# Optimization experiments

Measured on AMD Instinct MI355X. Metric: run time of the kernel, lower is better.

## Reference

```python
import jax, jax.numpy as jnp
import numpy as np

B, C, P, H, W = 8, 256, 64, 64, 64


def conv2d(x, w, b, pad):
    y = jax.lax.conv_general_dilated(
        x, w, window_strides=(1, 1), padding=[(pad, pad), (pad, pad)],
        dimension_numbers=("NCHW", "OIHW", "NCHW"))
    return y + b[None, :, None, None]


def setup_inputs() -> dict:
    key = jax.random.key(0)
    ks = jax.random.split(key, 9)
    x = jax.random.normal(ks[0], (B, C, H, W), dtype=jnp.float32)
    # conv weights, OIHW layout; scale ~ kaiming-ish
    w_top = jax.random.normal(ks[1], (P, C, 1, 1), jnp.float32) * (1.0 / np.sqrt(C))
    b_top = jnp.zeros((P,), jnp.float32)
    w_center = jax.random.normal(ks[2], (P, C, 1, 1), jnp.float32) * (1.0 / np.sqrt(C))
    b_center = jnp.zeros((P,), jnp.float32)
    w_bottom = jax.random.normal(ks[3], (C, C, 3, 3), jnp.float32) * (1.0 / np.sqrt(9 * C))
    b_bottom = jnp.zeros((C,), jnp.float32)
    w_out = jax.random.normal(ks[4], (C, C, 3, 3), jnp.float32) * (1.0 / np.sqrt(9 * C))
    b_out = jnp.zeros((C,), jnp.float32)
    return {"x": x, "w_top": w_top, "b_top": b_top, "w_center": w_center,
            "b_center": b_center, "w_bottom": w_bottom, "b_bottom": b_bottom,
            "w_out": w_out, "b_out": b_out}


def reference(x, w_top, b_top, w_center, b_center, w_bottom, b_bottom, w_out, b_out):
    b, c, h, w = x.shape
    hw = h * w
    x_top = conv2d(x, w_top, b_top, 0).reshape(b, -1, hw)          # [B, P, HW]
    x_center = conv2d(x, w_center, b_center, 0).reshape(b, -1, hw)  # [B, P, HW]
    x_center = jnp.swapaxes(x_center, 1, 2)                          # [B, HW, P]
    x_bottom = conv2d(x, w_bottom, b_bottom, 1).reshape(b, c, hw)
    x_bottom = jnp.swapaxes(x_bottom, 1, 2)                          # [B, HW, C]
    sp_map = jnp.einsum("bnp,bpm->bnm", x_center, x_top)            # [B, HW, HW]
    # NOTE: softmax is GLOBAL over the flattened HW*HW map per batch element,
    # not per-row (faithful to original Softmax(dim=1) on view(bsize, -1)).
    sp_map = jax.nn.softmax(sp_map.reshape(b, -1), axis=1).reshape(b, hw, hw)
    sp_map = jnp.einsum("bnm,bmc->bnc", sp_map, x_bottom)           # [B, HW, C]
    # NOTE: original does .reshape(b, C, h, w) on a [B, HW, C] tensor (no
    # transpose) -- replicate that exact memory reinterpretation.
    sp_map = sp_map.reshape(b, c, h, w)
    return conv2d(x + sp_map, w_out, b_out, 1)
```

## Files before the change

kernel.cpp:

```cpp
#include <hip/hip_runtime.h>
#include <hip/hip_bf16.h>
#include <type_traits>

constexpr int B_ = 8, C_ = 256, P_ = 64, H_ = 64, W_ = 64, HW_ = 4096;

typedef __attribute__((ext_vector_type(8))) short short8;
typedef __attribute__((ext_vector_type(4))) short short4v;
typedef __attribute__((ext_vector_type(4))) float f32x4;

__device__ __forceinline__ short bfbits(float f) {
    __hip_bfloat16 h = __float2bfloat16(f);
    return *reinterpret_cast<short*>(&h);
}
__device__ __forceinline__ float bf2f(short s) {
    __hip_bfloat16 h = *reinterpret_cast<__hip_bfloat16*>(&s);
    return (float)h;
}

#define GLL16(gsrc, ldst)                                                      \
    __builtin_amdgcn_global_load_lds(                                         \
        (const __attribute__((address_space(1))) void*)(gsrc),                \
        (__attribute__((address_space(3))) void*)(ldst), 16, 0, 0)


__global__ __launch_bounds__(256) void k_prep_w(
    const float* __restrict__ w, short8* __restrict__ wbP)
{
    const int idx = blockIdx.x * 256 + threadIdx.x;
    const int lane = idx & 63, cot = (idx >> 6) & 15;
    const int cb = (idx >> 10) & 7, tap = idx >> 13;
    const int lm = lane & 15, lq = lane >> 4;
    const int co = cot * 16 + lm, ci0 = cb * 32 + lq * 8;
    short8 v;
#pragma unroll
    for (int k = 0; k < 8; ++k)
        v[k] = bfbits(w[(co * 256 + ci0 + k) * 9 + tap]);
    wbP[idx] = v;
}

__global__ __launch_bounds__(256) void k_pack_xb(
    const __hip_bfloat16* __restrict__ xb, short8* __restrict__ xbP)
{
    const int tid = blockIdx.x * 256 + threadIdx.x;
    const int lane = tid & 63, wid = tid >> 6;
    const int ct = wid & 15, g = (wid >> 4) & 127, b = wid >> 11;
    const int c = ct * 16 + (lane >> 2);
    const int mo = g * 32 + (lane & 3) * 8;
    const short8 v = *reinterpret_cast<const short8*>(
        &xb[((size_t)(b * 256 + c)) * HW_ + mo]);
    xbP[(size_t)wid * 64 + (lane & 3) * 16 + (lane >> 2)] = v;
}

__global__ __launch_bounds__(256) void k_conv1x1(
    const float* __restrict__ x,
    const float* __restrict__ w_top, const float* __restrict__ b_top,
    const float* __restrict__ w_cen, const float* __restrict__ b_cen,
    short8* __restrict__ xtPh, short8* __restrict__ xtPl,
    short8* __restrict__ xcPh, short8* __restrict__ xcPl)
{
    const int b = blockIdx.z;
    const int n = blockIdx.x * 256 + threadIdx.x;
    const int conv = blockIdx.y >> 2, pq = blockIdx.y & 3;
    const int p0 = pq * 16;
    const float* w    = conv ? w_cen : w_top;
    const float* bias = conv ? b_cen : b_top;
    short8* oh = conv ? xcPh : xtPh;
    short8* ol = conv ? xcPl : xtPl;

    const float* xp = x + (size_t)b * C_ * HW_ + n;
    float acc[16];
#pragma unroll
    for (int p = 0; p < 16; ++p) acc[p] = 0.f;

    for (int c = 0; c < C_; c += 4) {
        const float xv0 = xp[(size_t)(c + 0) * HW_];
        const float xv1 = xp[(size_t)(c + 1) * HW_];
        const float xv2 = xp[(size_t)(c + 2) * HW_];
        const float xv3 = xp[(size_t)(c + 3) * HW_];
#pragma unroll
        for (int p = 0; p < 16; ++p) {
            const float4 wv = *reinterpret_cast<const float4*>(&w[(p0 + p) * C_ + c]);
            float a = acc[p];
            a = fmaf(wv.x, xv0, a);
            a = fmaf(wv.y, xv1, a);
            a = fmaf(wv.z, xv2, a);
            a = fmaf(wv.w, xv3, a);
            acc[p] = a;
        }
    }
    const int nt = n >> 4, lmn = n & 15;
    const size_t obase = ((size_t)(b * 256 + nt) * 2 + (pq >> 1)) * 64 + lmn;
#pragma unroll
    for (int jj = 0; jj < 2; ++jj) {
        short8 vh, vl;
#pragma unroll
        for (int k = 0; k < 8; ++k) {
            const float v = acc[jj * 8 + k] + bias[p0 + jj * 8 + k];
            const short hb = bfbits(v);
            vh[k] = hb;
            vl[k] = bfbits(v - bf2f(hb));
        }
        const size_t idx = obase + (size_t)(((pq & 1) * 2 + jj) * 16);
        oh[idx] = vh;
        ol[idx] = vl;
    }
}

template <typename OT>
__global__ __launch_bounds__(256) void k_conv3x3_mfma(
    const float* __restrict__ xin, const short8* __restrict__ wbP,
    const float* __restrict__ bias, OT* __restrict__ out)
{
    __shared__ __align__(16) __hip_bfloat16 Xs[3][66][40];
    const int b = blockIdx.z, h = blockIdx.x, cohalf = blockIdx.y;
    const int t = threadIdx.x;
    const int wave = t >> 6, lane = t & 63;
    const int lm = lane & 15, lq = lane >> 4;
    const int cobase = cohalf * 128 + wave * 32;
    const int cot0 = cohalf * 8 + wave * 2;

    f32x4 acc[4][2];
#pragma unroll
    for (int i = 0; i < 4; ++i)
#pragma unroll
        for (int j = 0; j < 2; ++j) acc[i][j] = f32x4{0.f, 0.f, 0.f, 0.f};

    if (t < 192) {
        const int r = t >> 6, cc = t & 31, side = (t >> 5) & 1;
        Xs[r][side ? 65 : 0][cc] = __float2bfloat16(0.f);
    }

    const int ci_ld = t & 31;
    const int grp   = t >> 5;
    const float* xbase = xin + (size_t)b * C_ * HW_;

    for (int cb = 0; cb < 8; ++cb) {
        const int ci0 = cb * 32;
        __syncthreads();
#pragma unroll
        for (int it = 0; it < 6; ++it) {
            const int qr = it * 8 + grp;
            const int r = qr >> 4, wq = qr & 15;
            const int hh = h + r - 1;
            float4 v = {0.f, 0.f, 0.f, 0.f};
            if (hh >= 0 && hh < H_)
                v = *reinterpret_cast<const float4*>(
                    &xbase[(size_t)(ci0 + ci_ld) * HW_ + hh * W_ + wq * 4]);
            Xs[r][1 + wq * 4 + 0][ci_ld] = __float2bfloat16(v.x);
            Xs[r][1 + wq * 4 + 1][ci_ld] = __float2bfloat16(v.y);
            Xs[r][1 + wq * 4 + 2][ci_ld] = __float2bfloat16(v.z);
            Xs[r][1 + wq * 4 + 3][ci_ld] = __float2bfloat16(v.w);
        }
        __syncthreads();

        for (int tap = 0; tap < 9; ++tap) {
            const int dh = tap / 3;
            const int dw = tap % 3;
            short8 bf[4];
#pragma unroll
            for (int nt = 0; nt < 4; ++nt)
                bf[nt] = *reinterpret_cast<const short8*>(
                    &Xs[dh][nt * 16 + lm + dw][lq * 8]);
            const short8* wp = wbP + ((size_t)(tap * 8 + cb)) * 1024 + lane;
            short8 af[2];
            af[0] = wp[(cot0 + 0) * 64];
            af[1] = wp[(cot0 + 1) * 64];
#pragma unroll
            for (int nt = 0; nt < 4; ++nt)
#pragma unroll
                for (int ct = 0; ct < 2; ++ct)
                    acc[nt][ct] = __builtin_amdgcn_mfma_f32_16x16x32_bf16(
                        af[ct], bf[nt], acc[nt][ct], 0, 0, 0);
        }
    }

#pragma unroll
    for (int nt = 0; nt < 4; ++nt) {
        const int pos = h * W_ + nt * 16 + lm;
#pragma unroll
        for (int ct = 0; ct < 2; ++ct) {
            const int co = cobase + ct * 16 + lq * 4;
#pragma unroll
            for (int r = 0; r < 4; ++r) {
                const float v = acc[nt][ct][r] + bias[co + r];
                if constexpr (std::is_same<OT, __hip_bfloat16>::value)
                    out[((size_t)(b * C_ + co + r)) * HW_ + pos] = __float2bfloat16(v);
                else
                    out[((size_t)(b * C_ + co + r)) * HW_ + pos] = v;
            }
        }
    }
}

__global__ __launch_bounds__(512, 2) void k_attn_mfma(
    const short8* __restrict__ xtPh, const short8* __restrict__ xtPl,
    const short8* __restrict__ xcPh, const short8* __restrict__ xcPl,
    const short8* __restrict__ xbP, float* __restrict__ O,
    float* __restrict__ Z)
{
    extern __shared__ __align__(16) char smem[];
    short8* XTs = (short8*)smem;
    short8* XBs = (short8*)(smem + 32768);
    short8* Ps8 = (short8*)(smem + 98304);
    short4v* Ps4 = (short4v*)(smem + 98304);
    float* zred = (float*)(smem + 114688);

    const int lin = blockIdx.x;
    const int b = lin & 7, nblk = lin >> 3;
    const int n0 = nblk * 128;

    const int t = threadIdx.x, wv = t >> 6, lane = t & 63;
    const int lm = lane & 15, lq = lane >> 4;
    const int mh = wv >> 2, nq2 = wv & 3;
    const int nq = wv >> 2, cq = wv & 3;

    short8 cB2[2][2][2];
#pragma unroll
    for (int ntile = 0; ntile < 2; ++ntile) {
        const int gt = nblk * 8 + nq2 * 2 + ntile;
        const size_t base = ((size_t)(b * 256 + gt) * 2) * 64 + lane;
        cB2[ntile][0][0] = xcPh[base];
        cB2[ntile][1][0] = xcPh[base + 64];
        cB2[ntile][0][1] = xcPl[base];
        cB2[ntile][1][1] = xcPl[base + 64];
    }
    asm volatile("s_waitcnt vmcnt(0)" ::: "memory");

    auto stage = [&](int smt, int bufi) {
        short8* XT = XTs + bufi * 1024;
        short8* XB = XBs + bufi * 2048;
        const size_t abase = ((size_t)(b * 512 + smt * 8)) * 64;
#pragma unroll
        for (int k = 0; k < 2; ++k) {
            const int c = wv * 2 + k, ms = c >> 2, part = c & 3;
            const short8* src = (part < 2 ? xtPh : xtPl)
                                + abase + ms * 128 + (part & 1) * 64 + lane;
            GLL16(src, XT + c * 64);
        }
        const size_t p8 = ((size_t)(b * 2048 + smt * 32)) * 64;
#pragma unroll
        for (int k = 0; k < 4; ++k) {
            const int e = k * 512 + wv * 64;
            GLL16(xbP + p8 + e + lane, XB + e);
        }
    };
    stage(0, 0);

    f32x4 acc[4][4];
#pragma unroll
    for (int i = 0; i < 4; ++i)
#pragma unroll
        for (int jj = 0; jj < 4; ++jj) acc[i][jj] = f32x4{0.f, 0.f, 0.f, 0.f};
    float zp = 0.f;

    for (int mt = 0; mt < 64; ++mt) {
        const int cur = mt & 1;
        asm volatile("s_waitcnt vmcnt(4)" ::: "memory");
        __builtin_amdgcn_sched_barrier(0);
        __builtin_amdgcn_s_barrier();
        __builtin_amdgcn_sched_barrier(0);
        stage((mt + 1) & 63, cur ^ 1);

        const short8* XT = XTs + cur * 1024;
#pragma unroll
        for (int ms2 = 0; ms2 < 2; ++ms2) {
            const int ms = mh * 2 + ms2;
            const short8 aH0 = XT[(ms * 4 + 0) * 64 + lane];
            const short8 aH1 = XT[(ms * 4 + 1) * 64 + lane];
            const short8 aL0 = XT[(ms * 4 + 2) * 64 + lane];
            const short8 aL1 = XT[(ms * 4 + 3) * 64 + lane];
#pragma unroll
            for (int ntile = 0; ntile < 2; ++ntile) {
                f32x4 s = {0.f, 0.f, 0.f, 0.f};
                __builtin_amdgcn_s_setprio(1);
                s = __builtin_amdgcn_mfma_f32_16x16x32_bf16(aH0, cB2[ntile][0][0], s, 0, 0, 0);
                s = __builtin_amdgcn_mfma_f32_16x16x32_bf16(aH1, cB2[ntile][1][0], s, 0, 0, 0);
                s = __builtin_amdgcn_mfma_f32_16x16x32_bf16(aH0, cB2[ntile][0][1], s, 0, 0, 0);
                s = __builtin_amdgcn_mfma_f32_16x16x32_bf16(aH1, cB2[ntile][1][1], s, 0, 0, 0);
                s = __builtin_amdgcn_mfma_f32_16x16x32_bf16(aL0, cB2[ntile][0][0], s, 0, 0, 0);
                s = __builtin_amdgcn_mfma_f32_16x16x32_bf16(aL1, cB2[ntile][1][0], s, 0, 0, 0);
                __builtin_amdgcn_s_setprio(0);
                const float e0 = __expf(s[0]), e1 = __expf(s[1]);
                const float e2 = __expf(s[2]), e3 = __expf(s[3]);
                zp += (e0 + e1) + (e2 + e3);
                short4v pk = { bfbits(e0), bfbits(e1), bfbits(e2), bfbits(e3) };
                const int T = nq2 * 2 + ntile;
                const int lqp = (ms & 1) * 2 + (lq >> 1);
                Ps4[(((T * 2 + mh) * 64) + lqp * 16 + lm) * 2 + (lq & 1)] = pk;
            }
        }
        asm volatile("s_waitcnt vmcnt(6) lgkmcnt(0)" ::: "memory");
        __builtin_amdgcn_sched_barrier(0);
        __builtin_amdgcn_s_barrier();
        __builtin_amdgcn_sched_barrier(0);

        const short8* XB = XBs + cur * 2048;
        short8 vb0[4], vb1[4];
#pragma unroll
        for (int q4 = 0; q4 < 4; ++q4) {
            const int ct = cq * 4 + q4;
            vb0[q4] = XB[ct * 64 + lane];
            vb1[q4] = XB[1024 + ct * 64 + lane];
        }
#pragma unroll
        for (int nt2 = 0; nt2 < 4; ++nt2) {
            const int T = nq * 4 + nt2;
            const short8 pa0 = Ps8[(T * 2 + 0) * 64 + lane];
            const short8 pa1 = Ps8[(T * 2 + 1) * 64 + lane];
            __builtin_amdgcn_s_setprio(1);
#pragma unroll
            for (int q4 = 0; q4 < 4; ++q4) {
                acc[nt2][q4] = __builtin_amdgcn_mfma_f32_16x16x32_bf16(
                    pa0, vb0[q4], acc[nt2][q4], 0, 0, 0);
                acc[nt2][q4] = __builtin_amdgcn_mfma_f32_16x16x32_bf16(
                    pa1, vb1[q4], acc[nt2][q4], 0, 0, 0);
            }
            __builtin_amdgcn_s_setprio(0);
        }
    }

#pragma unroll
    for (int o = 32; o > 0; o >>= 1) zp += __shfl_down(zp, o, 64);
    if (lane == 0) zred[wv] = zp;
    __syncthreads();
    if (t == 0) {
        float zs = 0.f;
#pragma unroll
        for (int wvi = 0; wvi < 8; ++wvi) zs += zred[wvi];
        atomicAdd(&Z[b], zs);
    }

#pragma unroll
    for (int nt2 = 0; nt2 < 4; ++nt2) {
#pragma unroll
        for (int q4 = 0; q4 < 4; ++q4) {
            const int c = cq * 64 + q4 * 16 + lm;
#pragma unroll
            for (int r = 0; r < 4; ++r) {
                const int n = n0 + (nq * 4 + nt2) * 16 + lq * 4 + r;
                O[((size_t)b * HW_ + n) * C_ + c] = acc[nt2][q4][r];
            }
        }
    }
}

__global__ __launch_bounds__(256) void k_add(
    const float* __restrict__ x, const float* __restrict__ o,
    const float* __restrict__ Z, float* __restrict__ y)
{
    const int bidx = blockIdx.x;
    const float invZ = 1.0f / Z[bidx >> 10];
    const size_t i = ((size_t)bidx * 256 + threadIdx.x) * 4;
    const float4 a = *reinterpret_cast<const float4*>(&x[i]);
    const float4 b = *reinterpret_cast<const float4*>(&o[i]);
    float4 r{fmaf(b.x, invZ, a.x), fmaf(b.y, invZ, a.y),
             fmaf(b.z, invZ, a.z), fmaf(b.w, invZ, a.w)};
    *reinterpret_cast<float4*>(&y[i]) = r;
}

extern "C" void kernel_launch(void* const* d_in, const int* in_sizes, int n_in,
                              void* d_out, int out_size, void* d_ws, size_t ws_size,
                              hipStream_t stream)
{
    const float* x   = (const float*)d_in[0];
    const float* wt  = (const float*)d_in[1];
    const float* bt  = (const float*)d_in[2];
    const float* wc  = (const float*)d_in[3];
    const float* bc  = (const float*)d_in[4];
    const float* wbo = (const float*)d_in[5];
    const float* bbo = (const float*)d_in[6];
    const float* wo  = (const float*)d_in[7];
    const float* bo  = (const float*)d_in[8];
    float* out = (float*)d_out;

    uint8_t* w8 = (uint8_t*)d_ws;
    const size_t MB = 1u << 20;
    short8* xtPh = (short8*)(w8);
    short8* xtPl = (short8*)(w8 + 4 * MB);
    short8* xcPh = (short8*)(w8 + 8 * MB);
    short8* xcPl = (short8*)(w8 + 12 * MB);
    __hip_bfloat16* xbB = (__hip_bfloat16*)(w8 + 16 * MB);
    short8* xbP  = (short8*)(w8 + 32 * MB);
    float*  O    = (float*)(w8 + 48 * MB);
    short8* Wb1  = (short8*)(w8 + 48 * MB);
    short8* Wb2  = (short8*)(w8 + 32 * MB);
    float*  y    = (float*)(w8);
    float*  Z    = (float*)(w8 + 80 * MB);

    hipMemsetAsync(Z, 0, B_ * sizeof(float), stream);
    k_prep_w<<<dim3(288), 256, 0, stream>>>(wbo, Wb1);
    k_conv1x1<<<dim3(16, 8, 8), 256, 0, stream>>>(x, wt, bt, wc, bc,
                                                  xtPh, xtPl, xcPh, xcPl);
    k_conv3x3_mfma<__hip_bfloat16><<<dim3(64, 2, 8), 256, 0, stream>>>(x, Wb1, bbo, xbB);
    k_pack_xb<<<dim3(4096), 256, 0, stream>>>(xbB, xbP);
    k_attn_mfma<<<dim3(256), dim3(512), 114720, stream>>>(xtPh, xtPl, xcPh, xcPl,
                                                          xbP, O, Z);
    k_prep_w<<<dim3(288), 256, 0, stream>>>(wo, Wb2);
    k_add<<<dim3(8192), 256, 0, stream>>>(x, O, Z, y);
    k_conv3x3_mfma<float><<<dim3(64, 2, 8), 256, 0, stream>>>(y, Wb2, bo, out);
}
```

Baseline: 399.9 us.

## Merge output-channel halves into 512-thread conv3x3 blocks sharing one input tile

Each conv3x3 block now has 8 waves and covers all 256 output channels of a row, where before two 4-wave blocks each covered 128. The staged input tile is therefore loaded and converted once per row instead of twice, which halves global reads and LDS fills for the input. The grid is flattened with batch as the fastest index, and the tap loop is partially unrolled with weight loads issued before the LDS reads. In exchange, the block is larger and may need more registers under the new launch bounds, and the grid has half as many blocks.

```diff
diff --git a/kernel.cpp b/kernel.cpp
--- a/kernel.cpp
+++ b/kernel.cpp
@@ -107,17 +107,18 @@
 }
 
 template <typename OT>
-__global__ __launch_bounds__(256) void k_conv3x3_mfma(
+__global__ __launch_bounds__(512, 4) void k_conv3x3_mfma(
     const float* __restrict__ xin, const short8* __restrict__ wbP,
     const float* __restrict__ bias, OT* __restrict__ out)
 {
     __shared__ __align__(16) __hip_bfloat16 Xs[3][66][40];
-    const int b = blockIdx.z, h = blockIdx.x, cohalf = blockIdx.y;
+    const int lin = blockIdx.x;
+    const int b = lin & 7, h = lin >> 3;
     const int t = threadIdx.x;
     const int wave = t >> 6, lane = t & 63;
     const int lm = lane & 15, lq = lane >> 4;
-    const int cobase = cohalf * 128 + wave * 32;
-    const int cot0 = cohalf * 8 + wave * 2;
+    const int cobase = wave * 32;
+    const int cot0 = wave * 2;
 
     f32x4 acc[4][2];
 #pragma unroll
@@ -130,41 +131,40 @@
         Xs[r][side ? 65 : 0][cc] = __float2bfloat16(0.f);
     }
 
-    const int ci_ld = t & 31;
-    const int grp   = t >> 5;
     const float* xbase = xin + (size_t)b * C_ * HW_;
 
     for (int cb = 0; cb < 8; ++cb) {
         const int ci0 = cb * 32;
         __syncthreads();
 #pragma unroll
-        for (int it = 0; it < 6; ++it) {
-            const int qr = it * 8 + grp;
-            const int r = qr >> 4, wq = qr & 15;
+        for (int it = 0; it < 3; ++it) {
+            const int idx = it * 512 + t;
+            const int r = idx >> 9, ci = (idx >> 4) & 31, wq = idx & 15;
             const int hh = h + r - 1;
             float4 v = {0.f, 0.f, 0.f, 0.f};
             if (hh >= 0 && hh < H_)
                 v = *reinterpret_cast<const float4*>(
-                    &xbase[(size_t)(ci0 + ci_ld) * HW_ + hh * W_ + wq * 4]);
-            Xs[r][1 + wq * 4 + 0][ci_ld] = __float2bfloat16(v.x);
-            Xs[r][1 + wq * 4 + 1][ci_ld] = __float2bfloat16(v.y);
-            Xs[r][1 + wq * 4 + 2][ci_ld] = __float2bfloat16(v.z);
-            Xs[r][1 + wq * 4 + 3][ci_ld] = __float2bfloat16(v.w);
+                    &xbase[(size_t)(ci0 + ci) * HW_ + hh * W_ + wq * 4]);
+            Xs[r][1 + wq * 4 + 0][ci] = __float2bfloat16(v.x);
+            Xs[r][1 + wq * 4 + 1][ci] = __float2bfloat16(v.y);
+            Xs[r][1 + wq * 4 + 2][ci] = __float2bfloat16(v.z);
+            Xs[r][1 + wq * 4 + 3][ci] = __float2bfloat16(v.w);
         }
         __syncthreads();
 
+#pragma unroll 3
         for (int tap = 0; tap < 9; ++tap) {
             const int dh = tap / 3;
             const int dw = tap % 3;
-            short8 bf[4];
-#pragma unroll
-            for (int nt = 0; nt < 4; ++nt)
-                bf[nt] = *reinterpret_cast<const short8*>(
-                    &Xs[dh][nt * 16 + lm + dw][lq * 8]);
             const short8* wp = wbP + ((size_t)(tap * 8 + cb)) * 1024 + lane;
             short8 af[2];
             af[0] = wp[(cot0 + 0) * 64];
             af[1] = wp[(cot0 + 1) * 64];
+            short8 bf[4];
+#pragma unroll
+            for (int nt = 0; nt < 4; ++nt)
+                bf[nt] = *reinterpret_cast<const short8*>(
+                    &Xs[dh][nt * 16 + lm + dw][lq * 8]);
 #pragma unroll
             for (int nt = 0; nt < 4; ++nt)
 #pragma unroll
@@ -391,11 +391,11 @@
     k_prep_w<<<dim3(288), 256, 0, stream>>>(wbo, Wb1);
     k_conv1x1<<<dim3(16, 8, 8), 256, 0, stream>>>(x, wt, bt, wc, bc,
                                                   xtPh, xtPl, xcPh, xcPl);
-    k_conv3x3_mfma<__hip_bfloat16><<<dim3(64, 2, 8), 256, 0, stream>>>(x, Wb1, bbo, xbB);
+    k_conv3x3_mfma<__hip_bfloat16><<<dim3(512), 512, 0, stream>>>(x, Wb1, bbo, xbB);
     k_pack_xb<<<dim3(4096), 256, 0, stream>>>(xbB, xbP);
     k_attn_mfma<<<dim3(256), dim3(512), 114720, stream>>>(xtPh, xtPl, xcPh, xcPl,
                                                           xbP, O, Z);
     k_prep_w<<<dim3(288), 256, 0, stream>>>(wo, Wb2);
     k_add<<<dim3(8192), 256, 0, stream>>>(x, O, Z, y);
-    k_conv3x3_mfma<float><<<dim3(64, 2, 8), 256, 0, stream>>>(y, Wb2, bo, out);
-}
+    k_conv3x3_mfma<float><<<dim3(512), 512, 0, stream>>>(y, Wb2, bo, out);
+}
```

Measured after the change: 386.7 us. 1.03x faster.
